# Optimization experiments

Measured on AMD Instinct MI355X. Metric: run time of the kernel, lower is better.

## Reference

```python
import jax, jax.numpy as jnp
import numpy as np

NUM_CLASSES = 81
THRESHOLD = 0.5
NEGPOS_RATIO = 3
ALPHA = 1.0
VAR0, VAR1 = 0.1, 0.2  # cfg['variance']
B, P, NOBJ = 64, 8732, 16


def setup_inputs() -> dict:
    key = jax.random.key(0)
    k1, k2, k3, k4, k5, k6, k7 = jax.random.split(key, 7)
    loc_data = jax.random.normal(k1, (B, P, 4), jnp.float32)
    conf_data = jax.random.normal(k2, (B, P, NUM_CLASSES), jnp.float32)
    # priors in center form (cx, cy, w, h), all in (0,1)
    centers = jax.random.uniform(k3, (P, 2), minval=0.05, maxval=0.95)
    sizes = jax.random.uniform(k4, (P, 2), minval=0.05, maxval=0.5)
    priors = jnp.concatenate([centers, sizes], axis=1).astype(jnp.float32)
    # targets: [B, NOBJ, 5] = (x1, y1, x2, y2, label), valid boxes with x1<x2
    tl = jax.random.uniform(k5, (B, NOBJ, 2), maxval=0.6)
    wh = jax.random.uniform(k6, (B, NOBJ, 2), minval=0.05, maxval=0.35)
    labels = jax.random.randint(k7, (B, NOBJ, 1), 0, NUM_CLASSES - 1).astype(jnp.float32)
    targets = jnp.concatenate([tl, tl + wh, labels], axis=2)
    return {"loc_data": loc_data, "conf_data": conf_data, "priors": priors, "targets": targets}


def point_form(boxes):
    # (cx,cy,w,h) -> (x1,y1,x2,y2)
    return jnp.concatenate([boxes[:, :2] - boxes[:, 2:] / 2,
                            boxes[:, :2] + boxes[:, 2:] / 2], axis=1)


def jaccard(a, b):
    # a: [n,4], b: [m,4], point form -> IoU [n,m]
    tl = jnp.maximum(a[:, None, :2], b[None, :, :2])
    br = jnp.minimum(a[:, None, 2:], b[None, :, 2:])
    wh = jnp.clip(br - tl, 0.0)
    inter = wh[..., 0] * wh[..., 1]
    area_a = ((a[:, 2] - a[:, 0]) * (a[:, 3] - a[:, 1]))[:, None]
    area_b = ((b[:, 2] - b[:, 0]) * (b[:, 3] - b[:, 1]))[None, :]
    return inter / (area_a + area_b - inter)


def encode(matched, priors):
    # matched: [P,4] point form GT, priors: [P,4] center form
    g_cxcy = (matched[:, :2] + matched[:, 2:]) / 2 - priors[:, :2]
    g_cxcy = g_cxcy / (VAR0 * priors[:, 2:])
    g_wh = jnp.log((matched[:, 2:] - matched[:, :2]) / priors[:, 2:]) / VAR1
    return jnp.concatenate([g_cxcy, g_wh], axis=1)


def match_one(truths, labels, priors):
    # truths: [NOBJ,4] point form, labels: [NOBJ]
    overlaps = jaccard(truths, point_form(priors))  # [NOBJ, P]
    best_prior_idx = jnp.argmax(overlaps, axis=1)   # [NOBJ]
    best_truth_overlap = jnp.max(overlaps, axis=0)  # [P]
    best_truth_idx = jnp.argmax(overlaps, axis=0)   # [P]
    # ensure every GT keeps its best prior
    best_truth_overlap = best_truth_overlap.at[best_prior_idx].set(2.0)
    best_truth_idx = best_truth_idx.at[best_prior_idx].set(jnp.arange(truths.shape[0]))
    matched = truths[best_truth_idx]                        # [P,4]
    conf = (labels[best_truth_idx] + 1).astype(jnp.int32)   # [P]
    conf = jnp.where(best_truth_overlap < THRESHOLD, 0, conf)
    return encode(matched, priors), conf


def smooth_l1(x):
    ax = jnp.abs(x)
    return jnp.where(ax < 1.0, 0.5 * x * x, ax - 0.5)


def reference(loc_data, conf_data, priors, targets):
    truths = targets[..., :4]
    labels = targets[..., 4]
    loc_t, conf_t = jax.vmap(match_one, in_axes=(0, 0, None))(truths, labels, priors)
    loc_t = jax.lax.stop_gradient(loc_t)  # targets are non-grad in the original
    pos = conf_t > 0                       # [B,P]
    num_pos = pos.sum(axis=1)              # [B]
    # localization loss (smooth L1, sum over positives)
    loss_l = jnp.sum(smooth_l1(loc_data - loc_t) * pos[..., None].astype(loc_data.dtype))
    # per-prior CE = logsumexp(logits) - logit[target]
    lse = jax.nn.logsumexp(conf_data, axis=2)                                   # [B,P]
    gathered = jnp.take_along_axis(conf_data, conf_t[..., None], axis=2)[..., 0]
    loss_c = lse - gathered                                                      # [B,P]
    # hard negative mining: rank negatives by loss, keep top 3*num_pos
    loss_c_mine = jnp.where(pos, 0.0, loss_c)
    idx_rank = jnp.argsort(jnp.argsort(-loss_c_mine, axis=1), axis=1)
    num_neg = jnp.minimum(NEGPOS_RATIO * num_pos, P - 1)
    neg = idx_rank < num_neg[:, None]
    sel = jnp.logical_or(pos, neg)
    loss_conf = jnp.sum(jnp.where(sel, loss_c, 0.0))
    N = num_pos.sum().astype(loc_data.dtype)
    return ALPHA * loss_l / N + loss_conf / N
```

## Files before the change

### kernel.cpp

```cpp
#include <hip/hip_runtime.h>

#define BB 64
#define PP 8732
#define NOBJ 16
#define NC 81
#define THRESH 0.5f
#define NEGPOS 3
#define NCHUNK 4
#define CHUNK (PP / NCHUNK)

#define TK_THREADS 512
#define TK_KEYS 18

__device__ __forceinline__ float smooth_l1(float x) {
    float ax = fabsf(x);
    return (ax < 1.0f) ? 0.5f * x * x : ax - 0.5f;
}

__global__ __launch_bounds__(256) void k_match(
    const float* __restrict__ loc_data, const float* __restrict__ priors,
    const float* __restrict__ targets,
    unsigned char* __restrict__ conf_t,
    int* __restrict__ num_pos_part, float* __restrict__ lloss_part,
    int* __restrict__ done_cnt, double* __restrict__ accum)
{
    const int chunk = blockIdx.x;
    const int b = blockIdx.y;
    const int tid = threadIdx.x;

    __shared__ float s_tx1[NOBJ], s_ty1[NOBJ], s_tx2[NOBJ], s_ty2[NOBJ];
    __shared__ float s_lab[NOBJ], s_area[NOBJ];
    __shared__ unsigned long long s_best[NOBJ];
    __shared__ int s_bpi[NOBJ];

    if (tid < NOBJ) {
        const float* t = targets + ((size_t)b * NOBJ + tid) * 5;
        float x1 = t[0], y1 = t[1], x2 = t[2], y2 = t[3];
        s_tx1[tid] = x1; s_ty1[tid] = y1; s_tx2[tid] = x2; s_ty2[tid] = y2;
        s_lab[tid] = t[4];
        s_area[tid] = (x2 - x1) * (y2 - y1);
        s_best[tid] = 0ull;
    }
    if (chunk == 0 && b == 0 && tid == 0) {
        accum[0] = 0.0; accum[1] = 0.0; done_cnt[0] = 0;
    }
    __syncthreads();

    unsigned long long best[NOBJ];
    #pragma unroll
    for (int t = 0; t < NOBJ; ++t) best[t] = 0ull;

    for (int p = tid; p < PP; p += 256) {
        float4 pr = ((const float4*)priors)[p];
        float px1 = pr.x - pr.z * 0.5f, py1 = pr.y - pr.w * 0.5f;
        float px2 = pr.x + pr.z * 0.5f, py2 = pr.y + pr.w * 0.5f;
        float pa = (px2 - px1) * (py2 - py1);
        unsigned revp = 0xFFFFFFFFu - (unsigned)p;
        #pragma unroll
        for (int t = 0; t < NOBJ; ++t) {
            float ix1 = fmaxf(s_tx1[t], px1), iy1 = fmaxf(s_ty1[t], py1);
            float ix2 = fminf(s_tx2[t], px2), iy2 = fminf(s_ty2[t], py2);
            float iw = fmaxf(ix2 - ix1, 0.f), ih = fmaxf(iy2 - iy1, 0.f);
            float inter = iw * ih;
            float iou = inter / (s_area[t] + pa - inter);
            unsigned long long key =
                ((unsigned long long)__float_as_uint(iou) << 32) | revp;
            if (key > best[t]) best[t] = key;
        }
    }
    #pragma unroll
    for (int t = 0; t < NOBJ; ++t) {
        unsigned long long v = best[t];
        for (int o = 32; o > 0; o >>= 1) {
            unsigned long long w = __shfl_down(v, o);
            if (w > v) v = w;
        }
        if ((tid & 63) == 0) atomicMax(&s_best[t], v);
    }
    __syncthreads();
    if (tid < NOBJ)
        s_bpi[tid] = (int)(0xFFFFFFFFu - (unsigned)(s_best[tid] & 0xFFFFFFFFull));
    __syncthreads();

    int n_pos = 0;
    float lloss = 0.f;
    const int p0 = chunk * CHUNK, p1 = p0 + CHUNK;
    for (int p = p0 + tid; p < p1; p += 256) {
        float4 pr = ((const float4*)priors)[p];
        float px1 = pr.x - pr.z * 0.5f, py1 = pr.y - pr.w * 0.5f;
        float px2 = pr.x + pr.z * 0.5f, py2 = pr.y + pr.w * 0.5f;
        float pa = (px2 - px1) * (py2 - py1);
        float bt_ov = -1.f;
        int bt_idx = 0;
        #pragma unroll
        for (int t = 0; t < NOBJ; ++t) {
            float ix1 = fmaxf(s_tx1[t], px1), iy1 = fmaxf(s_ty1[t], py1);
            float ix2 = fminf(s_tx2[t], px2), iy2 = fminf(s_ty2[t], py2);
            float iw = fmaxf(ix2 - ix1, 0.f), ih = fmaxf(iy2 - iy1, 0.f);
            float inter = iw * ih;
            float iou = inter / (s_area[t] + pa - inter);
            if (iou > bt_ov) { bt_ov = iou; bt_idx = t; }
        }
        #pragma unroll
        for (int i = 0; i < NOBJ; ++i)
            if (s_bpi[i] == p) { bt_idx = i; bt_ov = 2.0f; }

        int c = (bt_ov < THRESH) ? 0 : ((int)s_lab[bt_idx] + 1);
        conf_t[(size_t)b * PP + p] = (unsigned char)c;

        if (c > 0) {
            n_pos++;
            float mx1 = s_tx1[bt_idx], my1 = s_ty1[bt_idx];
            float mx2 = s_tx2[bt_idx], my2 = s_ty2[bt_idx];
            float gcx = ((mx1 + mx2) * 0.5f - pr.x) / (0.1f * pr.z);
            float gcy = ((my1 + my2) * 0.5f - pr.y) / (0.1f * pr.w);
            float gw = logf((mx2 - mx1) / pr.z) / 0.2f;
            float gh = logf((my2 - my1) / pr.w) / 0.2f;
            float4 ld = ((const float4*)loc_data)[(size_t)b * PP + p];
            lloss += smooth_l1(ld.x - gcx) + smooth_l1(ld.y - gcy) +
                     smooth_l1(ld.z - gw) + smooth_l1(ld.w - gh);
        }
    }

    for (int o = 32; o > 0; o >>= 1) {
        n_pos += __shfl_down(n_pos, o);
        lloss += __shfl_down(lloss, o);
    }
    __shared__ int s_np[4];
    __shared__ float s_ll[4];
    if ((tid & 63) == 0) { s_np[tid >> 6] = n_pos; s_ll[tid >> 6] = lloss; }
    __syncthreads();
    if (tid == 0) {
        num_pos_part[b * NCHUNK + chunk] = s_np[0] + s_np[1] + s_np[2] + s_np[3];
        lloss_part[b * NCHUNK + chunk] = s_ll[0] + s_ll[1] + s_ll[2] + s_ll[3];
    }
}

__global__ __launch_bounds__(256) void k_conf(
    const float* __restrict__ conf_data, const unsigned char* __restrict__ conf_t,
    float* __restrict__ lcm, double* __restrict__ accum)
{
    __shared__ float4 s_buf4[2][648];
    const int tid = threadIdx.x;
    const int r = tid >> 3;
    const int s = tid & 7;
    const int seg_start = s * 10;
    const int seg_len = (s == 7) ? 11 : 10;
    const int base_row = blockIdx.x * 256;
    const float4* g4base = (const float4*)conf_data;

    float4 t0, t1, t2;
    {
        const float4* g4 = g4base + (size_t)base_row * NC / 4;
        t0 = g4[tid]; t1 = g4[tid + 256];
        if (tid < 136) t2 = g4[tid + 512];
    }

    float posl = 0.f;
    for (int h = 0; h < 8; ++h) {
        float4* buf = s_buf4[h & 1];
        buf[tid] = t0; buf[tid + 256] = t1;
        if (tid < 136) buf[tid + 512] = t2;
        if (h + 1 < 8) {
            const float4* g4 = g4base + (size_t)(base_row + (h + 1) * 32) * NC / 4;
            t0 = g4[tid]; t1 = g4[tid + 256];
            if (tid < 136) t2 = g4[tid + 512];
        }
        __syncthreads();

        const float* myrow = (const float*)buf + r * NC;
        float v[11];
        #pragma unroll
        for (int j = 0; j < 11; ++j) v[j] = myrow[seg_start + j];

        float m = -1e30f;
        #pragma unroll
        for (int j = 0; j < 11; ++j) m = fmaxf(m, (j < seg_len) ? v[j] : -1e30f);
        m = fmaxf(m, __shfl_xor(m, 1));
        m = fmaxf(m, __shfl_xor(m, 2));
        m = fmaxf(m, __shfl_xor(m, 4));
        float e = 0.f;
        #pragma unroll
        for (int j = 0; j < 11; ++j) e += (j < seg_len) ? __expf(v[j] - m) : 0.f;
        e += __shfl_xor(e, 1);
        e += __shfl_xor(e, 2);
        e += __shfl_xor(e, 4);

        if (s == 0) {
            int row = base_row + h * 32 + r;
            int c = (int)conf_t[row];
            float lse = m + __logf(e);
            float lc = lse - myrow[c];
            bool pos = c > 0;
            lcm[row] = pos ? 0.f : lc;
            if (pos) posl += lc;
        }
    }
    for (int o = 32; o > 0; o >>= 1) posl += __shfl_down(posl, o);
    __shared__ float s_w[4];
    if ((tid & 63) == 0) s_w[tid >> 6] = posl;
    __syncthreads();
    if (tid == 0)
        atomicAdd(&accum[1], (double)(s_w[0] + s_w[1] + s_w[2] + s_w[3]));
}

__global__ __launch_bounds__(TK_THREADS) void k_topk(
    const float* __restrict__ lcm, const int* __restrict__ num_pos_part,
    const float* __restrict__ lloss_part,
    double* __restrict__ accum, int* __restrict__ done_cnt,
    float* __restrict__ out)
{
    const int b = blockIdx.x, tid = threadIdx.x;
    unsigned key[TK_KEYS];
    #pragma unroll
    for (int j = 0; j < TK_KEYS; ++j) {
        int i = tid + j * TK_THREADS;
        key[j] = (i < PP) ? __float_as_uint(lcm[(size_t)b * PP + i]) : 0u;
    }
    __shared__ int s_hist[256];
    __shared__ int s_vk[2];
    int np = num_pos_part[b * NCHUNK + 0] + num_pos_part[b * NCHUNK + 1] +
             num_pos_part[b * NCHUNK + 2] + num_pos_part[b * NCHUNK + 3];
    int k = NEGPOS * np;
    if (k > PP - 1) k = PP - 1;

    unsigned P = 0;
    int kk = k;
    #pragma unroll
    for (int rd = 0; rd < 4; ++rd) {
        const int shift = 24 - 8 * rd;
        if (tid < 256) s_hist[tid] = 0;
        __syncthreads();
        const unsigned hi_mask = (rd == 0) ? 0u : (0xFFFFFFFFu << (shift + 8));
        #pragma unroll
        for (int j = 0; j < TK_KEYS; ++j) {
            int i = tid + j * TK_THREADS;
            if (i < PP && (((key[j] ^ P) & hi_mask) == 0u))
                atomicAdd(&s_hist[(key[j] >> shift) & 255], 1);
        }
        __syncthreads();
        if (tid < 64) {
            int h0 = s_hist[4 * tid + 0], h1 = s_hist[4 * tid + 1];
            int h2 = s_hist[4 * tid + 2], h3 = s_hist[4 * tid + 3];
            int s3 = h3, s2 = h2 + s3, s1 = h1 + s2, s0 = h0 + s1;
            int acc = s0;
            #pragma unroll
            for (int o = 1; o < 64; o <<= 1) {
                int t = __shfl_down(acc, o);
                if (tid + o < 64) acc += t;
            }
            int excl = acc - s0;
            int c0 = s0 + excl, c1 = s1 + excl, c2 = s2 + excl, c3 = s3 + excl;
            unsigned long long m = __ballot(c0 >= kk);
            int L = 63 - __clzll(m);
            if (tid == L) {
                int vi, cnext;
                if (c3 >= kk)      { vi = 3; cnext = excl; }
                else if (c2 >= kk) { vi = 2; cnext = c3; }
                else if (c1 >= kk) { vi = 1; cnext = c2; }
                else               { vi = 0; cnext = c1; }
                s_vk[0] = 4 * tid + vi;
                s_vk[1] = kk - cnext;
            }
        }
        __syncthreads();
        P |= ((unsigned)s_vk[0]) << shift;
        kk = s_vk[1];
        __syncthreads();
    }

    const unsigned T = P;
    float sum = 0.f;
    int cgt = 0;
    #pragma unroll
    for (int j = 0; j < TK_KEYS; ++j) {
        if (key[j] > T) { sum += __uint_as_float(key[j]); cgt++; }
    }
    for (int o = 32; o > 0; o >>= 1) {
        sum += __shfl_down(sum, o);
        cgt += __shfl_down(cgt, o);
    }
    __shared__ float s_s[8];
    __shared__ int s_c[8];
    if ((tid & 63) == 0) { s_s[tid >> 6] = sum; s_c[tid >> 6] = cgt; }
    __syncthreads();
    if (tid == 0) {
        float tot = 0.f; int ctot = 0;
        for (int w = 0; w < 8; ++w) { tot += s_s[w]; ctot += s_c[w]; }
        float neg = tot + (float)(k - ctot) * __uint_as_float(T);
        atomicAdd(&accum[1], (double)neg);
        __threadfence();
        int prev = atomicAdd(done_cnt, 1);
        if (prev == BB - 1) {
            double a1 = atomicAdd(&accum[1], 0.0);
            int N = 0;
            double ll = 0.0;
            for (int i = 0; i < BB * NCHUNK; ++i) {
                N += num_pos_part[i];
                ll += (double)lloss_part[i];
            }
            out[0] = (float)((ll + a1) / (double)N);
        }
    }
}

extern "C" void kernel_launch(void* const* d_in, const int* in_sizes, int n_in,
                              void* d_out, int out_size, void* d_ws, size_t ws_size,
                              hipStream_t stream) {
    const float* loc_data  = (const float*)d_in[0];
    const float* conf_data = (const float*)d_in[1];
    const float* priors    = (const float*)d_in[2];
    const float* targets   = (const float*)d_in[3];

    char* ws = (char*)d_ws;
    double* accum = (double*)ws;
    int* done_cnt = (int*)(ws + 16);
    int* num_pos_part = (int*)(ws + 32);
    float* lloss_part = (float*)(ws + 1056);
    unsigned char* conf_t = (unsigned char*)(ws + 2560);
    float* lcm = (float*)(ws + 2560 + (size_t)BB * PP);


    dim3 mg(NCHUNK, BB);
    k_match<<<mg, 256, 0, stream>>>(loc_data, priors, targets, conf_t,
                                    num_pos_part, lloss_part, done_cnt, accum);

    k_conf<<<(BB * PP) / 256, 256, 0, stream>>>(conf_data, conf_t, lcm, accum);

    k_topk<<<BB, TK_THREADS, 0, stream>>>(lcm, num_pos_part, lloss_part,
                                          accum, done_cnt, (float*)d_out);
}
```

Before: 360.6 us.

## Split prior matching and fuse per-prior assignment into confidence kernel

```diff
diff --git a/kernel.cpp b/kernel.cpp
--- a/kernel.cpp
+++ b/kernel.cpp
@@ -8,6 +8,7 @@
 #define NEGPOS 3
 #define NCHUNK 4
 #define CHUNK (PP / NCHUNK)
+#define NBLK 2183
 
 #define TK_THREADS 512
 #define TK_KEYS 18
@@ -17,32 +18,29 @@
     return (ax < 1.0f) ? 0.5f * x * x : ax - 0.5f;
 }
 
-__global__ __launch_bounds__(256) void k_match(
-    const float* __restrict__ loc_data, const float* __restrict__ priors,
-    const float* __restrict__ targets,
-    unsigned char* __restrict__ conf_t,
-    int* __restrict__ num_pos_part, float* __restrict__ lloss_part,
-    int* __restrict__ done_cnt, double* __restrict__ accum)
+__global__ __launch_bounds__(256) void k_matchA(
+    const float* __restrict__ priors, const float* __restrict__ targets,
+    unsigned long long* __restrict__ g_best_part,
+    double* __restrict__ accum, int* __restrict__ nsum,
+    int* __restrict__ done_cnt)
 {
     const int chunk = blockIdx.x;
     const int b = blockIdx.y;
     const int tid = threadIdx.x;
 
     __shared__ float s_tx1[NOBJ], s_ty1[NOBJ], s_tx2[NOBJ], s_ty2[NOBJ];
-    __shared__ float s_lab[NOBJ], s_area[NOBJ];
+    __shared__ float s_area[NOBJ];
     __shared__ unsigned long long s_best[NOBJ];
-    __shared__ int s_bpi[NOBJ];
 
     if (tid < NOBJ) {
         const float* t = targets + ((size_t)b * NOBJ + tid) * 5;
         float x1 = t[0], y1 = t[1], x2 = t[2], y2 = t[3];
         s_tx1[tid] = x1; s_ty1[tid] = y1; s_tx2[tid] = x2; s_ty2[tid] = y2;
-        s_lab[tid] = t[4];
         s_area[tid] = (x2 - x1) * (y2 - y1);
         s_best[tid] = 0ull;
     }
     if (chunk == 0 && b == 0 && tid == 0) {
-        accum[0] = 0.0; accum[1] = 0.0; done_cnt[0] = 0;
+        accum[0] = 0.0; nsum[0] = 0; done_cnt[0] = 0;
     }
     __syncthreads();
 
@@ -50,7 +48,8 @@
     #pragma unroll
     for (int t = 0; t < NOBJ; ++t) best[t] = 0ull;
 
-    for (int p = tid; p < PP; p += 256) {
+    const int p0 = chunk * CHUNK, p1 = p0 + CHUNK;
+    for (int p = p0 + tid; p < p1; p += 256) {
         float4 pr = ((const float4*)priors)[p];
         float px1 = pr.x - pr.z * 0.5f, py1 = pr.y - pr.w * 0.5f;
         float px2 = pr.x + pr.z * 0.5f, py2 = pr.y + pr.w * 0.5f;
@@ -79,13 +78,64 @@
     }
     __syncthreads();
     if (tid < NOBJ)
-        s_bpi[tid] = (int)(0xFFFFFFFFu - (unsigned)(s_best[tid] & 0xFFFFFFFFull));
-    __syncthreads();
-
-    int n_pos = 0;
-    float lloss = 0.f;
-    const int p0 = chunk * CHUNK, p1 = p0 + CHUNK;
-    for (int p = p0 + tid; p < p1; p += 256) {
+        g_best_part[((size_t)b * NOBJ + tid) * NCHUNK + chunk] = s_best[tid];
+}
+
+__global__ __launch_bounds__(256) void k_conf_fused(
+    const float* __restrict__ loc_data, const float* __restrict__ conf_data,
+    const float* __restrict__ priors, const float* __restrict__ targets,
+    const unsigned long long* __restrict__ g_best_part,
+    float* __restrict__ lcm, float* __restrict__ llp_part,
+    int2* __restrict__ np_part)
+{
+    __shared__ float4 s_buf4[2][648];
+    __shared__ float s_tx1[2][NOBJ], s_ty1[2][NOBJ];
+    __shared__ float s_tx2[2][NOBJ], s_ty2[2][NOBJ];
+    __shared__ float s_lab[2][NOBJ], s_area[2][NOBJ];
+    __shared__ int s_bpi[2][NOBJ];
+    __shared__ int s_conf[256];
+    const int tid = threadIdx.x;
+    const int base_row = blockIdx.x * 256;
+    const int b0 = base_row / PP;
+    int split = (b0 + 1) * PP - base_row;
+    if (split > 256) split = 256;
+    const bool two = (split < 256);
+
+    if (tid < 32) {
+        int bt = tid >> 4, t = tid & 15;
+        if (bt == 0 || two) {
+            int gb = b0 + bt;
+            const float* tp = targets + ((size_t)gb * NOBJ + t) * 5;
+            float x1 = tp[0], y1 = tp[1], x2 = tp[2], y2 = tp[3];
+            s_tx1[bt][t] = x1; s_ty1[bt][t] = y1;
+            s_tx2[bt][t] = x2; s_ty2[bt][t] = y2;
+            s_lab[bt][t] = tp[4];
+            s_area[bt][t] = (x2 - x1) * (y2 - y1);
+            const unsigned long long* part =
+                g_best_part + ((size_t)gb * NOBJ + t) * NCHUNK;
+            unsigned long long m = part[0];
+            #pragma unroll
+            for (int c = 1; c < NCHUNK; ++c)
+                if (part[c] > m) m = part[c];
+            s_bpi[bt][t] = (int)(0xFFFFFFFFu - (unsigned)(m & 0xFFFFFFFFull));
+        }
+    }
+
+    const float4* g4base = (const float4*)conf_data;
+    float4 t0, t1, t2;
+    {
+        const float4* g4 = g4base + (size_t)base_row * NC / 4;
+        t0 = g4[tid]; t1 = g4[tid + 256];
+        if (tid < 136) t2 = g4[tid + 512];
+    }
+    __syncthreads();
+
+    const int seg = (tid < split) ? 0 : 1;
+    const int row = base_row + tid;
+    const int p = row - (b0 + seg) * PP;
+    float llp = 0.f;
+    int np0 = 0, np1 = 0;
+    {
         float4 pr = ((const float4*)priors)[p];
         float px1 = pr.x - pr.z * 0.5f, py1 = pr.y - pr.w * 0.5f;
         float px2 = pr.x + pr.z * 0.5f, py2 = pr.y + pr.w * 0.5f;
@@ -94,69 +144,40 @@
         int bt_idx = 0;
         #pragma unroll
         for (int t = 0; t < NOBJ; ++t) {
-            float ix1 = fmaxf(s_tx1[t], px1), iy1 = fmaxf(s_ty1[t], py1);
-            float ix2 = fminf(s_tx2[t], px2), iy2 = fminf(s_ty2[t], py2);
+            float ix1 = fmaxf(s_tx1[seg][t], px1), iy1 = fmaxf(s_ty1[seg][t], py1);
+            float ix2 = fminf(s_tx2[seg][t], px2), iy2 = fminf(s_ty2[seg][t], py2);
             float iw = fmaxf(ix2 - ix1, 0.f), ih = fmaxf(iy2 - iy1, 0.f);
             float inter = iw * ih;
-            float iou = inter / (s_area[t] + pa - inter);
+            float iou = inter / (s_area[seg][t] + pa - inter);
             if (iou > bt_ov) { bt_ov = iou; bt_idx = t; }
         }
         #pragma unroll
         for (int i = 0; i < NOBJ; ++i)
-            if (s_bpi[i] == p) { bt_idx = i; bt_ov = 2.0f; }
-
-        int c = (bt_ov < THRESH) ? 0 : ((int)s_lab[bt_idx] + 1);
-        conf_t[(size_t)b * PP + p] = (unsigned char)c;
+            if (s_bpi[seg][i] == p) { bt_idx = i; bt_ov = 2.0f; }
+
+        int c = (bt_ov < THRESH) ? 0 : ((int)s_lab[seg][bt_idx] + 1);
+        s_conf[tid] = c;
 
         if (c > 0) {
-            n_pos++;
-            float mx1 = s_tx1[bt_idx], my1 = s_ty1[bt_idx];
-            float mx2 = s_tx2[bt_idx], my2 = s_ty2[bt_idx];
+            if (seg == 0) np0 = 1; else np1 = 1;
+            float mx1 = s_tx1[seg][bt_idx], my1 = s_ty1[seg][bt_idx];
+            float mx2 = s_tx2[seg][bt_idx], my2 = s_ty2[seg][bt_idx];
             float gcx = ((mx1 + mx2) * 0.5f - pr.x) / (0.1f * pr.z);
             float gcy = ((my1 + my2) * 0.5f - pr.y) / (0.1f * pr.w);
             float gw = logf((mx2 - mx1) / pr.z) / 0.2f;
             float gh = logf((my2 - my1) / pr.w) / 0.2f;
-            float4 ld = ((const float4*)loc_data)[(size_t)b * PP + p];
-            lloss += smooth_l1(ld.x - gcx) + smooth_l1(ld.y - gcy) +
-                     smooth_l1(ld.z - gw) + smooth_l1(ld.w - gh);
-        }
-    }
-
-    for (int o = 32; o > 0; o >>= 1) {
-        n_pos += __shfl_down(n_pos, o);
-        lloss += __shfl_down(lloss, o);
-    }
-    __shared__ int s_np[4];
-    __shared__ float s_ll[4];
-    if ((tid & 63) == 0) { s_np[tid >> 6] = n_pos; s_ll[tid >> 6] = lloss; }
-    __syncthreads();
-    if (tid == 0) {
-        num_pos_part[b * NCHUNK + chunk] = s_np[0] + s_np[1] + s_np[2] + s_np[3];
-        lloss_part[b * NCHUNK + chunk] = s_ll[0] + s_ll[1] + s_ll[2] + s_ll[3];
-    }
-}
-
-__global__ __launch_bounds__(256) void k_conf(
-    const float* __restrict__ conf_data, const unsigned char* __restrict__ conf_t,
-    float* __restrict__ lcm, double* __restrict__ accum)
-{
-    __shared__ float4 s_buf4[2][648];
-    const int tid = threadIdx.x;
+            float4 ld = ((const float4*)loc_data)[row];
+            llp += smooth_l1(ld.x - gcx) + smooth_l1(ld.y - gcy) +
+                   smooth_l1(ld.z - gw) + smooth_l1(ld.w - gh);
+        }
+    }
+    __syncthreads();
+
     const int r = tid >> 3;
     const int s = tid & 7;
     const int seg_start = s * 10;
     const int seg_len = (s == 7) ? 11 : 10;
-    const int base_row = blockIdx.x * 256;
-    const float4* g4base = (const float4*)conf_data;
-
-    float4 t0, t1, t2;
-    {
-        const float4* g4 = g4base + (size_t)base_row * NC / 4;
-        t0 = g4[tid]; t1 = g4[tid + 256];
-        if (tid < 136) t2 = g4[tid + 512];
-    }
-
-    float posl = 0.f;
+
     for (int h = 0; h < 8; ++h) {
         float4* buf = s_buf4[h & 1];
         buf[tid] = t0; buf[tid + 256] = t1;
@@ -187,30 +208,60 @@
         e += __shfl_xor(e, 4);
 
         if (s == 0) {
-            int row = base_row + h * 32 + r;
-            int c = (int)conf_t[row];
+            int idx = h * 32 + r;
+            int c = s_conf[idx];
             float lse = m + __logf(e);
             float lc = lse - myrow[c];
             bool pos = c > 0;
-            lcm[row] = pos ? 0.f : lc;
-            if (pos) posl += lc;
-        }
-    }
-    for (int o = 32; o > 0; o >>= 1) posl += __shfl_down(posl, o);
-    __shared__ float s_w[4];
-    if ((tid & 63) == 0) s_w[tid >> 6] = posl;
-    __syncthreads();
-    if (tid == 0)
-        atomicAdd(&accum[1], (double)(s_w[0] + s_w[1] + s_w[2] + s_w[3]));
+            lcm[base_row + idx] = pos ? 0.f : lc;
+            if (pos) llp += lc;
+        }
+    }
+
+    for (int o = 32; o > 0; o >>= 1) {
+        llp += __shfl_down(llp, o);
+        np0 += __shfl_down(np0, o);
+        np1 += __shfl_down(np1, o);
+    }
+    __shared__ float s_l[4];
+    __shared__ int s_n0[4], s_n1[4];
+    if ((tid & 63) == 0) {
+        s_l[tid >> 6] = llp; s_n0[tid >> 6] = np0; s_n1[tid >> 6] = np1;
+    }
+    __syncthreads();
+    if (tid == 0) {
+        llp_part[blockIdx.x] = s_l[0] + s_l[1] + s_l[2] + s_l[3];
+        np_part[blockIdx.x] = make_int2(s_n0[0] + s_n0[1] + s_n0[2] + s_n0[3],
+                                        s_n1[0] + s_n1[1] + s_n1[2] + s_n1[3]);
+    }
 }
 
 __global__ __launch_bounds__(TK_THREADS) void k_topk(
-    const float* __restrict__ lcm, const int* __restrict__ num_pos_part,
-    const float* __restrict__ lloss_part,
-    double* __restrict__ accum, int* __restrict__ done_cnt,
-    float* __restrict__ out)
+    const float* __restrict__ lcm, const int2* __restrict__ np_part,
+    const float* __restrict__ llp_part,
+    double* __restrict__ accum, int* __restrict__ nsum,
+    int* __restrict__ done_cnt, float* __restrict__ out)
 {
     const int b = blockIdx.x, tid = threadIdx.x;
+
+    __shared__ int s_npb;
+    {
+        int gs = (b * PP) >> 8;
+        int ge = ((b + 1) * PP - 1) >> 8;
+        int cnt = ge - gs + 1;
+        int mynp = 0;
+        if (tid < cnt) {
+            int g = gs + tid;
+            int2 e = np_part[g];
+            int bg0 = (g << 8) / PP;
+            mynp = (bg0 == b) ? e.x : e.y;
+        }
+        if (tid < 64) {
+            for (int o = 32; o > 0; o >>= 1) mynp += __shfl_down(mynp, o);
+            if (tid == 0) s_npb = mynp;
+        }
+    }
+
     unsigned key[TK_KEYS];
     #pragma unroll
     for (int j = 0; j < TK_KEYS; ++j) {
@@ -219,8 +270,8 @@
     }
     __shared__ int s_hist[256];
     __shared__ int s_vk[2];
-    int np = num_pos_part[b * NCHUNK + 0] + num_pos_part[b * NCHUNK + 1] +
-             num_pos_part[b * NCHUNK + 2] + num_pos_part[b * NCHUNK + 3];
+    __syncthreads();
+    const int np = s_npb;
     int k = NEGPOS * np;
     if (k > PP - 1) k = PP - 1;
 
@@ -282,24 +333,34 @@
     }
     __shared__ float s_s[8];
     __shared__ int s_c[8];
+    __shared__ int s_last;
     if ((tid & 63) == 0) { s_s[tid >> 6] = sum; s_c[tid >> 6] = cgt; }
     __syncthreads();
     if (tid == 0) {
         float tot = 0.f; int ctot = 0;
         for (int w = 0; w < 8; ++w) { tot += s_s[w]; ctot += s_c[w]; }
         float neg = tot + (float)(k - ctot) * __uint_as_float(T);
-        atomicAdd(&accum[1], (double)neg);
+        atomicAdd(&accum[0], (double)neg);
+        atomicAdd(nsum, np);
         __threadfence();
-        int prev = atomicAdd(done_cnt, 1);
-        if (prev == BB - 1) {
-            double a1 = atomicAdd(&accum[1], 0.0);
-            int N = 0;
-            double ll = 0.0;
-            for (int i = 0; i < BB * NCHUNK; ++i) {
-                N += num_pos_part[i];
-                ll += (double)lloss_part[i];
-            }
-            out[0] = (float)((ll + a1) / (double)N);
+        s_last = (atomicAdd(done_cnt, 1) == BB - 1) ? 1 : 0;
+    }
+    __syncthreads();
+
+    if (s_last) {
+        double acc = 0.0;
+        for (int i = tid; i < NBLK; i += TK_THREADS)
+            acc += (double)llp_part[i];
+        for (int o = 32; o > 0; o >>= 1) acc += __shfl_down(acc, o);
+        __shared__ double s_d[8];
+        if ((tid & 63) == 0) s_d[tid >> 6] = acc;
+        __syncthreads();
+        if (tid == 0) {
+            double llp_tot = 0.0;
+            for (int w = 0; w < 8; ++w) llp_tot += s_d[w];
+            double neg_tot = atomicAdd(&accum[0], 0.0);
+            int N = atomicAdd(nsum, 0);
+            out[0] = (float)((llp_tot + neg_tot) / (double)N);
         }
     }
 }
@@ -314,19 +375,21 @@
 
     char* ws = (char*)d_ws;
     double* accum = (double*)ws;
-    int* done_cnt = (int*)(ws + 16);
-    int* num_pos_part = (int*)(ws + 32);
-    float* lloss_part = (float*)(ws + 1056);
-    unsigned char* conf_t = (unsigned char*)(ws + 2560);
-    float* lcm = (float*)(ws + 2560 + (size_t)BB * PP);
+    int* nsum = (int*)(ws + 8);
+    int* done_cnt = (int*)(ws + 12);
+    unsigned long long* g_best_part = (unsigned long long*)(ws + 512);
+    float* llp_part = (float*)(ws + 33280);
+    int2* np_part = (int2*)(ws + 42016);
+    float* lcm = (float*)(ws + 59488);
 
 
     dim3 mg(NCHUNK, BB);
-    k_match<<<mg, 256, 0, stream>>>(loc_data, priors, targets, conf_t,
-                                    num_pos_part, lloss_part, done_cnt, accum);
-
-    k_conf<<<(BB * PP) / 256, 256, 0, stream>>>(conf_data, conf_t, lcm, accum);
-
-    k_topk<<<BB, TK_THREADS, 0, stream>>>(lcm, num_pos_part, lloss_part,
-                                          accum, done_cnt, (float*)d_out);
-}
+    k_matchA<<<mg, 256, 0, stream>>>(priors, targets, g_best_part,
+                                     accum, nsum, done_cnt);
+
+    k_conf_fused<<<NBLK, 256, 0, stream>>>(loc_data, conf_data, priors, targets,
+                                           g_best_part, lcm, llp_part, np_part);
+
+    k_topk<<<BB, TK_THREADS, 0, stream>>>(lcm, np_part, llp_part,
+                                          accum, nsum, done_cnt, (float*)d_out);
+}
```

Measured after the change: 296.6 us. 17.8% less time.
